# Optimization experiments

Measured on AMD Instinct MI355X. Metric: run time of the kernel, lower is better.

## Reference

```python
import jax, jax.numpy as jnp
import numpy as np

HEAD_DIM = 128
N_HEADS = 16
N_KV_HEADS = 4
N_REP = N_HEADS // N_KV_HEADS


def _rope(x, cos, sin):
    # x: [B, S, Hk, D]; cos/sin: [S, D/2]
    xr = x.reshape(*x.shape[:-1], -1, 2)
    x0, x1 = xr[..., 0], xr[..., 1]
    c = cos[None, :, None, :]
    s = sin[None, :, None, :]
    o0 = x0 * c - x1 * s
    o1 = x0 * s + x1 * c
    return jnp.stack([o0, o1], axis=-1).reshape(x.shape)


def setup_inputs() -> dict:
    key = jax.random.key(0)
    ks = jax.random.split(key, 7)
    B, S, DIM = 2, 1024, 2048
    KV_DIM = HEAD_DIM * N_KV_HEADS
    x = jax.random.normal(ks[0], (B, S, DIM), dtype=jnp.float32)
    # rotary angles like LLaMA: freqs = 1/10000^(2i/D)
    inv_freq = 1.0 / (10000.0 ** (np.arange(0, HEAD_DIM, 2, dtype=np.float32) / HEAD_DIM))
    ang = np.arange(S, dtype=np.float32)[:, None] * inv_freq[None, :]  # [S, D/2]
    theta_cos = jnp.asarray(np.cos(ang))
    theta_sin = jnp.asarray(np.sin(ang))
    sc = 0.02
    wq = jax.random.normal(ks[1], (DIM, DIM), dtype=jnp.float32) * sc
    wk = jax.random.normal(ks[2], (DIM, KV_DIM), dtype=jnp.float32) * sc
    wv = jax.random.normal(ks[3], (DIM, KV_DIM), dtype=jnp.float32) * sc
    wo = jax.random.normal(ks[4], (DIM, DIM), dtype=jnp.float32) * sc
    return {"x": x, "theta_cos": theta_cos, "theta_sin": theta_sin,
            "wq": wq, "wk": wk, "wv": wv, "wo": wo}


def reference(x, theta_cos, theta_sin, wq, wk, wv, wo):
    B, S, DIM = x.shape
    # projections
    xq = (x @ wq).reshape(B, S, N_HEADS, HEAD_DIM).transpose(0, 2, 1, 3)  # [B,H,S,D]
    xk = (x @ wk).reshape(B, S, N_KV_HEADS, HEAD_DIM)                      # [B,S,Hk,D]
    xv = (x @ wv).reshape(B, S, N_KV_HEADS, HEAD_DIM)
    # RoPE on K and V only (faithful to source: Q is NOT rotated)
    xk = _rope(xk, theta_cos, theta_sin)
    xv = _rope(xv, theta_cos, theta_sin)
    # GQA repeat: [B,S,Hk,D] -> [B,H,S,D] (each kv head repeated consecutively)
    xk = jnp.repeat(xk.transpose(0, 2, 1, 3), N_REP, axis=1)
    xv = jnp.repeat(xv.transpose(0, 2, 1, 3), N_REP, axis=1)
    scale = HEAD_DIM ** (-0.5)
    att = jnp.einsum('bhqd,bhkd->bhqk', xq, xk) * scale
    # faithful masking: tril then masked_fill(att == 0, -inf)
    tri = jnp.tril(jnp.ones((S, S), dtype=bool))
    att = jnp.where(tri[None, None], att, 0.0)
    att = jnp.where(att == 0.0, -jnp.inf, att)
    att = jax.nn.softmax(att, axis=-1)
    y = jnp.einsum('bhqk,bhkd->bhqd', att, xv)
    out = y.transpose(0, 2, 1, 3).reshape(B, S, DIM)
    return out @ wo
```

## Files before the change

### kernel.cpp

```cpp
#include <hip/hip_runtime.h>
#include <hip/hip_bf16.h>
#include <stdint.h>
#include <math.h>

typedef _Float16 half_t;
typedef __attribute__((ext_vector_type(2))) _Float16 h2_t;
typedef __attribute__((ext_vector_type(4))) _Float16 h4_t;
typedef __attribute__((ext_vector_type(8))) _Float16 h8_t;
typedef __attribute__((ext_vector_type(4))) float f32x4;
typedef __attribute__((ext_vector_type(4))) uint32_t u32x4;

#if __has_builtin(__builtin_amdgcn_exp2f)
#define EXP2(x) __builtin_amdgcn_exp2f(x)
#else
#define EXP2(x) exp2f(x)
#endif

__device__ __forceinline__ void gload16(const void* g, void* l) {
    __builtin_amdgcn_global_load_lds(
        (const __attribute__((address_space(1))) uint32_t*)(uintptr_t)g,
        (__attribute__((address_space(3))) uint32_t*)(uint32_t)(uintptr_t)l,
        16, 0, 0);
}

__global__ __launch_bounds__(256) void prep(const float* __restrict__ x, half_t* __restrict__ xh,
                                            const float* __restrict__ wq, const float* __restrict__ wk,
                                            const float* __restrict__ wv, const float* __restrict__ wo,
                                            half_t* __restrict__ qt, half_t* __restrict__ kt,
                                            half_t* __restrict__ vt, half_t* __restrict__ ot) {
    __shared__ half_t T[32][36];
    const int bx = blockIdx.x;
    if (bx < 2048) {
        int g = (bx * 256 + threadIdx.x) * 8;
        float4 a = *(const float4*)(x + g);
        float4 b = *(const float4*)(x + g + 4);
        h8_t o = {(half_t)a.x,(half_t)a.y,(half_t)a.z,(half_t)a.w,
                  (half_t)b.x,(half_t)b.y,(half_t)b.z,(half_t)b.w};
        *(h8_t*)(xh + g) = o;
        return;
    }
    const int wb = bx - 2048;
    const float* src; half_t* dst; int Nd, t;
    if (wb < 4096)      { src = wq; dst = qt; Nd = 2048; t = wb; }
    else if (wb < 5120) { src = wk; dst = kt; Nd = 512;  t = wb - 4096; }
    else if (wb < 6144) { src = wv; dst = vt; Nd = 512;  t = wb - 5120; }
    else                { src = wo; dst = ot; Nd = 2048; t = wb - 6144; }
    const int K = 2048;
    int nt = Nd >> 5;
    int ti = t / nt, tj = t % nt;
    int r  = threadIdx.x >> 3;
    int c4 = (threadIdx.x & 7) << 2;
    float4 v = *(const float4*)(src + (size_t)(ti*32 + r) * Nd + tj*32 + c4);
    T[r][c4+0] = (half_t)v.x; T[r][c4+1] = (half_t)v.y;
    T[r][c4+2] = (half_t)v.z; T[r][c4+3] = (half_t)v.w;
    __syncthreads();
    h4_t o = {T[c4+0][r], T[c4+1][r], T[c4+2][r], T[c4+3][r]};
    *(h4_t*)(dst + (size_t)(tj*32 + r) * K + ti*32 + c4) = o;
}

template<int BM, int QKV, typename CT>
__global__ __launch_bounds__(256) void gemm_t(const half_t* __restrict__ A,
                                              const half_t* __restrict__ Bq,
                                              const half_t* __restrict__ Bk,
                                              const half_t* __restrict__ Bv,
                                              CT* __restrict__ Cq,
                                              half_t* __restrict__ Ck,
                                              half_t* __restrict__ Cv,
                                              int NB, int K) {
    constexpr int MI  = BM / 32;
    constexpr int ACH = BM / 8;
    constexpr int TOT = ACH + 16;
    constexpr int PW  = TOT / 4;
    __shared__ half_t Ah[BM * 64];
    __shared__ half_t Bh[128 * 64];
    const int tid = threadIdx.x, lane = tid & 63, wid = tid >> 6;
    const int lr = lane & 15, lg = lane >> 4;
    const int wm = wid >> 1, wn = wid & 1;
    const int nwg = gridDim.x, bid = blockIdx.x;
    const int swz = (bid & 7) * (nwg >> 3) + (bid >> 3);
    const int bm = swz / NB, bn = swz % NB;
    const int m0 = bm * BM;

    const half_t* W; CT* Cc; int cs, col0;
    if constexpr (QKV) {
        if (bn < 16)      { W = Bq + (size_t)bn * 128 * K;        Cc = Cq;       cs = 2048; col0 = bn * 128; }
        else if (bn < 20) { W = Bk + (size_t)(bn - 16) * 128 * K; Cc = (CT*)Ck;  cs = 512;  col0 = (bn - 16) * 128; }
        else              { W = Bv + (size_t)(bn - 20) * 128 * K; Cc = (CT*)Cv;  cs = 512;  col0 = (bn - 20) * 128; }
    } else {
        W = Bq + (size_t)bn * 128 * K; Cc = Cq; cs = NB * 128; col0 = bn * 128;
    }

    const half_t* Arow = A + (size_t)m0 * K;
    f32x4 acc[MI][4] = {};

    for (int k0 = 0; k0 < K; k0 += 64) {
        #pragma unroll
        for (int c = 0; c < PW; c++) {
            const int chunk = wid * PW + c;
            const int o = lane * 16;
            if (chunk < ACH) {
                const int go   = (chunk << 10) + o;
                const int row  = go >> 7;
                const int colb = (go & 127) ^ ((row & 7) << 4);
                gload16(Arow + (size_t)row * K + k0 + (colb >> 1), (char*)Ah + (chunk << 10));
            } else {
                const int go   = ((chunk - ACH) << 10) + o;
                const int row  = go >> 7;
                const int colb = (go & 127) ^ ((row & 7) << 4);
                gload16(W + (size_t)row * K + k0 + (colb >> 1), (char*)Bh + ((chunk - ACH) << 10));
            }
        }
        __syncthreads();
        h8_t af[2][MI], bf[2][4];
        #pragma unroll
        for (int kk = 0; kk < 2; kk++) {
            #pragma unroll
            for (int mi = 0; mi < MI; mi++) {
                const int row = wm * (BM / 2) + mi * 16 + lr;
                const int cb  = (kk * 64 + lg * 16) ^ ((lr & 7) << 4);
                af[kk][mi] = *(const h8_t*)((const char*)Ah + row * 128 + cb);
            }
            #pragma unroll
            for (int ni = 0; ni < 4; ni++) {
                const int row = wn * 64 + ni * 16 + lr;
                const int cb  = (kk * 64 + lg * 16) ^ ((lr & 7) << 4);
                bf[kk][ni] = *(const h8_t*)((const char*)Bh + row * 128 + cb);
            }
        }
        #pragma unroll
        for (int kk = 0; kk < 2; kk++)
            #pragma unroll
            for (int mi = 0; mi < MI; mi++)
                #pragma unroll
                for (int ni = 0; ni < 4; ni++)
                    acc[mi][ni] = __builtin_amdgcn_mfma_f32_16x16x32_f16(af[kk][mi], bf[kk][ni], acc[mi][ni], 0, 0, 0);
        __syncthreads();
    }

    #pragma unroll
    for (int mi = 0; mi < MI; mi++)
        #pragma unroll
        for (int ni = 0; ni < 4; ni++)
            #pragma unroll
            for (int r = 0; r < 4; r++) {
                int row = m0 + wm * (BM / 2) + mi * 16 + lg * 4 + r;
                int col = col0 + wn * 64 + ni * 16 + lr;
                Cc[(size_t)row * cs + col] = (CT)acc[mi][ni][r];
            }
}

__global__ __launch_bounds__(256) void rope(half_t* __restrict__ Kh, const half_t* __restrict__ Vh,
                                            half_t* __restrict__ Vt, const float* __restrict__ cs,
                                            const float* __restrict__ sn) {
    const int bx = blockIdx.x;
    if (bx < 2048) {
        int gid = bx * 256 + threadIdx.x;
        int row = gid >> 8;
        int pc  = gid & 255;
        int s   = row & 1023;
        int p   = pc & 63;
        float c = cs[s * 64 + p], si = sn[s * 64 + p];
        h2_t v = *(h2_t*)(Kh + (size_t)row * 512 + 2 * pc);
        float x0 = (float)v[0], x1 = (float)v[1];
        h2_t o = {(half_t)(x0 * c - x1 * si), (half_t)(x0 * si + x1 * c)};
        *(h2_t*)(Kh + (size_t)row * 512 + 2 * pc) = o;
        return;
    }
    int gid = (bx - 2048) * 256 + threadIdx.x;
    int col = gid & 2047;
    int dp  = gid >> 11;
    int s   = col & 1023;
    int p   = dp & 63;
    float c = cs[s * 64 + p], si = sn[s * 64 + p];
    h2_t v = *(const h2_t*)(Vh + (size_t)col * 512 + 2 * dp);
    float x0 = (float)v[0], x1 = (float)v[1];
    Vt[(size_t)(2 * dp)     * 2048 + col] = (half_t)(x0 * c - x1 * si);
    Vt[(size_t)(2 * dp + 1) * 2048 + col] = (half_t)(x0 * si + x1 * c);
}

__global__ __launch_bounds__(256, 4) void attn8(const half_t* __restrict__ Qh,
                                                const half_t* __restrict__ Kh,
                                                const half_t* __restrict__ Vtg,
                                                half_t* __restrict__ Yh,
                                                half_t* __restrict__ Yp,
                                                float* __restrict__ ML) {
    __shared__ half_t K0[64 * 128];
    __shared__ half_t V0[128 * 64];

    const int tid = threadIdx.x, lane = tid & 63, wid = tid >> 6;
    const int lr = lane & 15, lg = lane >> 4;
    const int bx = blockIdx.x;
    const int g  = bx & 7;
    const int local = bx >> 3;
    const int b = g >> 2, kvh = g & 3;
    const int h = kvh * 4 + (local & 3);
    const int pp = local >> 2;
    int qt, kb0, kb1, part; bool partial;
    if (pp < 8)            { qt = 8 + pp;           kb0 = 0; kb1 = 7;  partial = true;  part = 0; }
    else if (!(pp & 1))    { qt = 7 - ((pp-8)>>1);  kb0 = 0; kb1 = qt; partial = false; part = 0; }
    else                   { qt = 15 - ((pp-9)>>1); kb0 = 8; kb1 = qt; partial = true;  part = 1; }

    const int qbase = qt * 64 + wid * 16;
    const int q     = qbase + lr;
    const size_t qrow0 = (size_t)(b * 1024 + qbase);
    const size_t kbase = (size_t)b * 1024;

    const float sc2 = 0.08838834764831845f * 1.4426950408889634f;
    h8_t qf[4];
    #pragma unroll
    for (int kk = 0; kk < 4; kk++) {
        qf[kk] = *(const h8_t*)(Qh + ((size_t)(b * 1024) + q) * 2048 + h * 128 + kk * 32 + lg * 8);
        qf[kk] = qf[kk] * (half_t)sc2;
    }

    float m = -1e30f, l = 0.f;
    f32x4 yacc[8] = {};

    for (int kb = kb0; kb <= kb1; kb++) {
        const int j = kb * 64;
        __syncthreads();
        #pragma unroll
        for (int c = 0; c < 4; c++) {
            const int chunk = wid * 4 + c;
            const int o = (chunk << 10) + lane * 16;
            { const int row  = o >> 8;
              const int colb = (o & 255) ^ ((row & 7) << 4);
              gload16(Kh + (kbase + j + row) * 512 + kvh * 128 + (colb >> 1),
                      (char*)K0 + (chunk << 10)); }
            { const int row  = o >> 7;
              const int colb = (o & 127) ^ ((row & 7) << 4);
              gload16(Vtg + (size_t)(kvh * 128 + row) * 2048 + kbase + j + (colb >> 1),
                      (char*)V0 + (chunk << 10)); }
        }
        __syncthreads();

        f32x4 st[4] = {};
        __builtin_amdgcn_s_setprio(1);
        #pragma unroll
        for (int t4 = 0; t4 < 4; t4++)
            #pragma unroll
            for (int kk = 0; kk < 4; kk++) {
                const int row = t4 * 16 + lr;
                const int cb  = (kk * 64 + lg * 16) ^ ((lr & 7) << 4);
                h8_t kf = *(const h8_t*)((const char*)K0 + row * 256 + cb);
                st[t4] = __builtin_amdgcn_mfma_f32_16x16x32_f16(kf, qf[kk], st[t4], 0, 0, 0);
            }
        __builtin_amdgcn_s_setprio(0);
        if (kb == qt) {
            #pragma unroll
            for (int t4 = 0; t4 < 4; t4++)
                #pragma unroll
                for (int r = 0; r < 4; r++)
                    if (j + t4 * 16 + lg * 4 + r > q) st[t4][r] = -1e30f;
        }
        float mb = fmaxf(fmaxf(fmaxf(st[0][0], st[0][1]), fmaxf(st[0][2], st[0][3])),
                         fmaxf(fmaxf(st[1][0], st[1][1]), fmaxf(st[1][2], st[1][3])));
        mb = fmaxf(mb, fmaxf(fmaxf(fmaxf(st[2][0], st[2][1]), fmaxf(st[2][2], st[2][3])),
                             fmaxf(fmaxf(st[3][0], st[3][1]), fmaxf(st[3][2], st[3][3]))));
        mb = fmaxf(mb, __shfl_xor(mb, 16));
        mb = fmaxf(mb, __shfl_xor(mb, 32));
        if (!__all(mb - m <= 8.0f)) {
            float mn = fmaxf(m, mb);
            float al = EXP2(m - mn);
            m = mn;
            l *= al;
            #pragma unroll
            for (int dt = 0; dt < 8; dt++)
                #pragma unroll
                for (int r = 0; r < 4; r++)
                    yacc[dt][r] *= al;
        }
        float rs = 0.f;
        #pragma unroll
        for (int t4 = 0; t4 < 4; t4++)
            #pragma unroll
            for (int r = 0; r < 4; r++) {
                float p = EXP2(st[t4][r] - m);
                st[t4][r] = p;
                rs += p;
            }
        rs += __shfl_xor(rs, 16);
        rs += __shfl_xor(rs, 32);
        l += rs;
        uint32_t h2p[4][2];
        #pragma unroll
        for (int t4 = 0; t4 < 4; t4++) {
            h2p[t4][0] = __builtin_bit_cast(uint32_t,
                __builtin_amdgcn_cvt_pkrtz(st[t4][0], st[t4][1]));
            h2p[t4][1] = __builtin_bit_cast(uint32_t,
                __builtin_amdgcn_cvt_pkrtz(st[t4][2], st[t4][3]));
        }
        const int src1 = ((lg & 1) << 5) + lr;
        const int src2 = src1 + 16;
        const bool sel = (lg < 2);
        h8_t pb[2];
        #pragma unroll
        for (int c = 0; c < 2; c++) {
            uint32_t lo0 = __shfl((int)h2p[2*c][0],   src1);
            uint32_t lo1 = __shfl((int)h2p[2*c][1],   src1);
            uint32_t lo2 = __shfl((int)h2p[2*c][0],   src2);
            uint32_t lo3 = __shfl((int)h2p[2*c][1],   src2);
            uint32_t hi0 = __shfl((int)h2p[2*c+1][0], src1);
            uint32_t hi1 = __shfl((int)h2p[2*c+1][1], src1);
            uint32_t hi2 = __shfl((int)h2p[2*c+1][0], src2);
            uint32_t hi3 = __shfl((int)h2p[2*c+1][1], src2);
            u32x4 w = { sel ? lo0 : hi0, sel ? lo1 : hi1,
                        sel ? lo2 : hi2, sel ? lo3 : hi3 };
            pb[c] = __builtin_bit_cast(h8_t, w);
        }
        __builtin_amdgcn_s_setprio(1);
        #pragma unroll
        for (int dt = 0; dt < 8; dt++) {
            const int row = dt * 16 + lr;
            const int cb0 = (lg * 16) ^ ((lr & 7) << 4);
            const int cb1 = (64 + lg * 16) ^ ((lr & 7) << 4);
            h8_t v0 = *(const h8_t*)((const char*)V0 + row * 128 + cb0);
            h8_t v1 = *(const h8_t*)((const char*)V0 + row * 128 + cb1);
            yacc[dt] = __builtin_amdgcn_mfma_f32_16x16x32_f16(v0, pb[0], yacc[dt], 0, 0, 0);
            yacc[dt] = __builtin_amdgcn_mfma_f32_16x16x32_f16(v1, pb[1], yacc[dt], 0, 0, 0);
        }
        __builtin_amdgcn_s_setprio(0);
    }

    const float inv = 1.0f / l;
    if (!partial) {
        #pragma unroll
        for (int dt = 0; dt < 8; dt++) {
            h4_t o = {(half_t)(yacc[dt][0] * inv), (half_t)(yacc[dt][1] * inv),
                      (half_t)(yacc[dt][2] * inv), (half_t)(yacc[dt][3] * inv)};
            *(h4_t*)(Yh + ((size_t)(b * 1024) + q) * 2048 + h * 128 + dt * 16 + lg * 4) = o;
        }
    } else {
        const int pidx = ((b * 16 + h) * 8 + (qt - 8)) * 2 + part;
        half_t* yp = Yp + (size_t)pidx * 8192;
        const int rl = wid * 16 + lr;
        #pragma unroll
        for (int dt = 0; dt < 8; dt++) {
            h4_t o = {(half_t)(yacc[dt][0] * inv), (half_t)(yacc[dt][1] * inv),
                      (half_t)(yacc[dt][2] * inv), (half_t)(yacc[dt][3] * inv)};
            *(h4_t*)(yp + rl * 128 + dt * 16 + lg * 4) = o;
        }
        if (lg == 0) {
            float* ml = ML + (size_t)pidx * 128;
            ml[rl]      = m;
            ml[64 + rl] = l;
        }
    }
}

__global__ __launch_bounds__(256) void merge2(const half_t* __restrict__ Yp,
                                              const float* __restrict__ ML,
                                              half_t* __restrict__ Yh) {
    const int sidx = blockIdx.x;
    const int b = sidx >> 7;
    const int rem = sidx & 127;
    const int h = rem >> 3;
    const int qt = 8 + (rem & 7);
    const int t = threadIdx.x;
    const int row = t >> 2;
    const int cg = (t & 3) * 32;
    const float* ml0 = ML + (size_t)(sidx * 2) * 128;
    const float* ml1 = ml0 + 128;
    const float m0 = ml0[row], l0 = ml0[64 + row];
    const float m1 = ml1[row], l1 = ml1[64 + row];
    const float M  = fmaxf(m0, m1);
    const float w0 = l0 * EXP2(m0 - M), w1 = l1 * EXP2(m1 - M);
    const float inv = 1.0f / (w0 + w1);
    const float a0 = w0 * inv, a1 = w1 * inv;
    const half_t* y0 = Yp + (size_t)(sidx * 2) * 8192 + row * 128 + cg;
    const half_t* y1 = y0 + 8192;
    half_t* out = Yh + ((size_t)(b * 1024 + qt * 64 + row)) * 2048 + h * 128 + cg;
    #pragma unroll
    for (int c = 0; c < 32; c += 8) {
        h8_t u = *(const h8_t*)(y0 + c);
        h8_t v = *(const h8_t*)(y1 + c);
        h8_t o;
        #pragma unroll
        for (int e = 0; e < 8; e++)
            o[e] = (half_t)(a0 * (float)u[e] + a1 * (float)v[e]);
        *(h8_t*)(out + c) = o;
    }
}

extern "C" void kernel_launch(void* const* d_in, const int* in_sizes, int n_in,
                              void* d_out, int out_size, void* d_ws, size_t ws_size,
                              hipStream_t stream) {
    const float* x  = (const float*)d_in[0];
    const float* tc = (const float*)d_in[1];
    const float* ts = (const float*)d_in[2];
    const float* wq = (const float*)d_in[3];
    const float* wk = (const float*)d_in[4];
    const float* wv = (const float*)d_in[5];
    const float* wo = (const float*)d_in[6];
    float* out = (float*)d_out;

    const size_t MD = 2048ull * 2048, MK = 2048ull * 512;
    half_t* Xh  = (half_t*)d_ws;
    half_t* Qh  = Xh  + MD;
    half_t* Kh  = Qh  + MD;
    half_t* Vh  = Kh  + MK;
    half_t* Vt  = Vh  + MK;
    half_t* Yh  = Vt  + MK;
    half_t* wqt = Yh  + MD;
    half_t* wkt = wqt + MD;
    half_t* wvt = wkt + MK;
    half_t* wot = wvt + MK;
    half_t* Yp  = wot + MD;
    float*  ML  = (float*)(Yp + 512ull * 8192);

    prep<<<12288, 256, 0, stream>>>(x, Xh, wq, wk, wv, wo, wqt, wkt, wvt, wot);
    gemm_t<64, 1, half_t><<<768, 256, 0, stream>>>(Xh, wqt, wkt, wvt, Qh, Kh, Vh, 24, 2048);
    rope<<<4096, 256, 0, stream>>>(Kh, Vh, Vt, tc, ts);
    attn8<<<768, 256, 0, stream>>>(Qh, Kh, Vt, Yh, Yp, ML);
    merge2<<<256, 256, 0, stream>>>(Yp, ML, Yh);
    gemm_t<64, 0, float><<<512, 256, 0, stream>>>(Yh, wot, nullptr, nullptr, out, nullptr, nullptr, 16, 2048);
}
```

Baseline: 119.4 us.

## Prefetch next K/V tile into registers during attention compute

The attention kernel now loads the first K/V tile to LDS before the loop. Each iteration issues global loads for the next tile into registers while the current tile's QK and PV MFMAs run, then writes them to LDS after a barrier. This aims to hide global memory latency that was previously exposed between the two barriers of each iteration. The register staging raises VGPR pressure, so launch bounds drop from 4 to 3 blocks per SM, which lowers occupancy.

```diff
diff --git a/kernel.cpp b/kernel.cpp
--- a/kernel.cpp
+++ b/kernel.cpp
@@ -178,7 +178,7 @@
     Vt[(size_t)(2 * dp + 1) * 2048 + col] = (half_t)(x0 * si + x1 * c);
 }
 
-__global__ __launch_bounds__(256, 4) void attn8(const half_t* __restrict__ Qh,
+__global__ __launch_bounds__(256, 3) void attn9(const half_t* __restrict__ Qh,
                                                 const half_t* __restrict__ Kh,
                                                 const half_t* __restrict__ Vtg,
                                                 half_t* __restrict__ Yh,
@@ -202,7 +202,6 @@
 
     const int qbase = qt * 64 + wid * 16;
     const int q     = qbase + lr;
-    const size_t qrow0 = (size_t)(b * 1024 + qbase);
     const size_t kbase = (size_t)b * 1024;
 
     const float sc2 = 0.08838834764831845f * 1.4426950408889634f;
@@ -216,9 +215,8 @@
     float m = -1e30f, l = 0.f;
     f32x4 yacc[8] = {};
 
-    for (int kb = kb0; kb <= kb1; kb++) {
-        const int j = kb * 64;
-        __syncthreads();
+    {
+        const int j = kb0 * 64;
         #pragma unroll
         for (int c = 0; c < 4; c++) {
             const int chunk = wid * 4 + c;
@@ -232,8 +230,28 @@
               gload16(Vtg + (size_t)(kvh * 128 + row) * 2048 + kbase + j + (colb >> 1),
                       (char*)V0 + (chunk << 10)); }
         }
-        __syncthreads();
-
+    }
+    __syncthreads();
+
+    for (int kb = kb0; kb <= kb1; kb++) {
+        const bool pf = (kb + 1 <= kb1);
+        h8_t kpre[4], vpre[4];
+        if (pf) {
+            const int j2 = (kb + 1) * 64;
+            #pragma unroll
+            for (int c = 0; c < 4; c++) {
+                const int chunk = wid * 4 + c;
+                const int o = (chunk << 10) + lane * 16;
+                { const int row  = o >> 8;
+                  const int colb = (o & 255) ^ ((row & 7) << 4);
+                  kpre[c] = *(const h8_t*)(Kh + (kbase + j2 + row) * 512 + kvh * 128 + (colb >> 1)); }
+                { const int row  = o >> 7;
+                  const int colb = (o & 127) ^ ((row & 7) << 4);
+                  vpre[c] = *(const h8_t*)(Vtg + (size_t)(kvh * 128 + row) * 2048 + kbase + j2 + (colb >> 1)); }
+            }
+        }
+
+        const int j = kb * 64;
         f32x4 st[4] = {};
         __builtin_amdgcn_s_setprio(1);
         #pragma unroll
@@ -320,6 +338,18 @@
             yacc[dt] = __builtin_amdgcn_mfma_f32_16x16x32_f16(v1, pb[1], yacc[dt], 0, 0, 0);
         }
         __builtin_amdgcn_s_setprio(0);
+
+        __syncthreads();
+        if (pf) {
+            #pragma unroll
+            for (int c = 0; c < 4; c++) {
+                const int chunk = wid * 4 + c;
+                const int o = (chunk << 10) + lane * 16;
+                *(h8_t*)((char*)K0 + o) = kpre[c];
+                *(h8_t*)((char*)V0 + o) = vpre[c];
+            }
+            __syncthreads();
+        }
     }
 
     const float inv = 1.0f / l;
@@ -411,7 +441,7 @@
     prep<<<12288, 256, 0, stream>>>(x, Xh, wq, wk, wv, wo, wqt, wkt, wvt, wot);
     gemm_t<64, 1, half_t><<<768, 256, 0, stream>>>(Xh, wqt, wkt, wvt, Qh, Kh, Vh, 24, 2048);
     rope<<<4096, 256, 0, stream>>>(Kh, Vh, Vt, tc, ts);
-    attn8<<<768, 256, 0, stream>>>(Qh, Kh, Vt, Yh, Yp, ML);
+    attn9<<<768, 256, 0, stream>>>(Qh, Kh, Vt, Yh, Yp, ML);
     merge2<<<256, 256, 0, stream>>>(Yp, ML, Yh);
     gemm_t<64, 0, float><<<512, 256, 0, stream>>>(Yh, wot, nullptr, nullptr, out, nullptr, nullptr, 16, 2048);
 }
```

Measured after the change: 118.8 us. No clear change (-0.5%).
